# Optimization experiments

Measured on AMD Instinct MI355X. Metric: run time of the kernel, lower is better.

The kernel has to match this reference:

```python
import jax, jax.numpy as jnp
import numpy as np


def setup_inputs() -> dict:
    key = jax.random.key(0)
    ks = jax.random.split(key, 10)
    B, L, Din, Dout = 64, 512, 256, 256
    s = 0.05
    inp = jax.random.normal(ks[0], (B, L, Din), jnp.float32)
    ci = jax.random.randint(ks[1], (B, L), 0, L)
    # valid coref indices: ci[:, i] must be in [0, i] (refers to an already-produced state)
    ci = ci % (jnp.arange(L) + 1)[None, :]
    p = lambda k, sh: jax.random.normal(k, sh, jnp.float32) * s
    return {
        "inp": inp,
        "last_coref_idx": ci,
        "Wr": p(ks[2], (Din, Dout)), "br": jnp.zeros((Dout,), jnp.float32),
        "Ur": p(ks[3], (Dout, Dout)),
        "Wz": p(ks[4], (Din, Dout)), "bz": jnp.zeros((Dout,), jnp.float32),
        "Uz": p(ks[5], (Dout, Dout)),
        "Wh": p(ks[6], (Din, Dout)), "bh": jnp.zeros((Dout,), jnp.float32),
        "Uh": p(ks[7], (Dout, Dout)),
        "k1": p(ks[8], (Din, 1)),
        "k2": p(ks[9], (Din, 1)),
    }


def reference(inp, last_coref_idx, Wr, br, Ur, Wz, bz, Uz, Wh, bh, Uh, k1, k2):
    B, L, Din = inp.shape
    Dout = Wr.shape[1]
    split = Dout // 2
    bidx = jnp.arange(B)

    def step(carry, xs):
        h_last, hist = carry            # h_last [B,Dout], hist [L,B,Dout]
        x, c, i = xs                    # x [B,Din], c [B] int, i scalar step index
        # coref = state_history[c-1][b] if c > 0 else zeros
        coref = hist[jnp.clip(c - 1, 0), bidx]
        coref = jnp.where((c > 0)[:, None], coref, jnp.zeros_like(coref))
        # attention between h_last-half and coref-half
        e = jnp.concatenate([x @ k1, x @ k2], axis=1)      # [B,2]
        a = jax.nn.softmax(e, axis=1)[:, 0:1]              # [B,1]
        mt = jnp.concatenate([a * h_last[:, :split], (1.0 - a) * coref[:, split:]], axis=1)
        r = jax.nn.sigmoid(x @ Wr + br + mt @ Ur)
        z = jax.nn.sigmoid(x @ Wz + bz + mt @ Uz)
        h_ = jnp.tanh(x @ Wh + bh + r * (mt @ Uh))
        h = (1.0 - z) * mt + z * h_
        hist = jax.lax.dynamic_update_index_in_dim(hist, h, i, 0)
        return (h, hist), h

    h0 = jnp.zeros((B, Dout), inp.dtype)
    hist0 = jnp.zeros((L, B, Dout), inp.dtype)
    xs = (jnp.swapaxes(inp, 0, 1), jnp.swapaxes(last_coref_idx, 0, 1), jnp.arange(L))
    _, ys = jax.lax.scan(step, (h0, hist0), xs)            # ys [L,B,Dout]
    return jnp.swapaxes(ys, 0, 1)                          # [B,L,Dout]
```

## Files before the change

### kernel.cpp

```cpp
#include <hip/hip_runtime.h>
#include <stdint.h>
#include <stddef.h>

typedef _Float16 half_t;
typedef _Float16 half2_t __attribute__((ext_vector_type(2)));
typedef _Float16 half8_t __attribute__((ext_vector_type(8)));
typedef float    floatx4 __attribute__((ext_vector_type(4)));
typedef uint32_t u32x4   __attribute__((ext_vector_type(4)));

#define SEQ_L 512
#define NBATCH 64
#define DIM 256
#define NTOT (NBATCH * SEQ_L)

__device__ __forceinline__ float fdot2f(uint32_t a, uint32_t b, float c) {
#if defined(__has_builtin)
#if __has_builtin(__builtin_amdgcn_fdot2)
  return __builtin_amdgcn_fdot2(__builtin_bit_cast(half2_t, a),
                                __builtin_bit_cast(half2_t, b), c, false);
#else
  half2_t av = __builtin_bit_cast(half2_t, a);
  half2_t bv = __builtin_bit_cast(half2_t, b);
  return c + (float)av[0] * (float)bv[0] + (float)av[1] * (float)bv[1];
#endif
#else
  half2_t av = __builtin_bit_cast(half2_t, a);
  half2_t bv = __builtin_bit_cast(half2_t, b);
  return c + (float)av[0] * (float)bv[0] + (float)av[1] * (float)bv[1];
#endif
}

__device__ __forceinline__ float sigmoidf_fast(float x) {
  return 1.0f / (1.0f + __expf(-x));
}
__device__ __forceinline__ float tanhf_fast(float x) {
  float e = __expf(2.0f * x);
  return 1.0f - 2.0f / (e + 1.0f);
}

__global__ void conv_w_kernel(const float* __restrict__ Wr,
                              const float* __restrict__ Wz,
                              const float* __restrict__ Wh,
                              half_t* __restrict__ Wt) {
  int n = blockIdx.x;
  int k = threadIdx.x;
  const float* W = (n < 256) ? Wr : ((n < 512) ? Wz : Wh);
  int j = n & 255;
  Wt[(size_t)n * DIM + k] = (half_t)W[(size_t)k * DIM + j];
}

__global__ __launch_bounds__(256) void attn_a_kernel(const float* __restrict__ inp,
                                                     const float* __restrict__ k1,
                                                     const float* __restrict__ k2,
                                                     float* __restrict__ a_arr) {
  int row  = blockIdx.x * 4 + (threadIdx.x >> 6);
  int lane = threadIdx.x & 63;
  const float4* x4 = (const float4*)(inp + (size_t)row * DIM);
  float4 xv  = x4[lane];
  float4 k1v = ((const float4*)k1)[lane];
  float4 k2v = ((const float4*)k2)[lane];
  float e1 = xv.x * k1v.x + xv.y * k1v.y + xv.z * k1v.z + xv.w * k1v.w;
  float e2 = xv.x * k2v.x + xv.y * k2v.y + xv.z * k2v.z + xv.w * k2v.w;
#pragma unroll
  for (int off = 32; off >= 1; off >>= 1) {
    e1 += __shfl_xor(e1, off);
    e2 += __shfl_xor(e2, off);
  }
  if (lane == 0) a_arr[row] = 1.0f / (1.0f + __expf(e2 - e1));
}

__global__ __launch_bounds__(256) void gemm_p_kernel(const float* __restrict__ X,
                                                     const half_t* __restrict__ Wt,
                                                     half_t* __restrict__ P) {
  __shared__ __align__(16) half_t As[128][32];
  __shared__ __align__(16) half_t Bs[128][32];
  const int tid  = threadIdx.x;
  const int bm   = blockIdx.x * 128;
  const int bn   = blockIdx.y * 128;
  const int lane = tid & 63;
  const int wave = tid >> 6;
  const int wm   = (wave >> 1) * 64;
  const int wn   = (wave & 1) * 64;
  const int quad = lane >> 4;
  const int l15  = lane & 15;
  const int r0   = tid >> 2;
  const int kc   = (tid & 3) * 8;

  floatx4 acc[4][4] = {};

  for (int k0 = 0; k0 < DIM; k0 += 32) {
#pragma unroll
    for (int hh = 0; hh < 2; ++hh) {
      int r = r0 + hh * 64;
      const float* asrc = X + (size_t)(bm + r) * DIM + k0 + kc;
      float4 f0 = *(const float4*)(asrc);
      float4 f1 = *(const float4*)(asrc + 4);
      half8_t av;
      av[0] = (half_t)f0.x; av[1] = (half_t)f0.y; av[2] = (half_t)f0.z; av[3] = (half_t)f0.w;
      av[4] = (half_t)f1.x; av[5] = (half_t)f1.y; av[6] = (half_t)f1.z; av[7] = (half_t)f1.w;
      *(half8_t*)(&As[r][kc]) = av;
      *(half8_t*)(&Bs[r][kc]) = *(const half8_t*)(Wt + (size_t)(bn + r) * DIM + k0 + kc);
    }
    __syncthreads();
    half8_t af[4], bf[4];
#pragma unroll
    for (int mi = 0; mi < 4; ++mi)
      af[mi] = *(const half8_t*)(&As[wm + mi * 16 + l15][quad * 8]);
#pragma unroll
    for (int ni = 0; ni < 4; ++ni)
      bf[ni] = *(const half8_t*)(&Bs[wn + ni * 16 + l15][quad * 8]);
#pragma unroll
    for (int mi = 0; mi < 4; ++mi)
#pragma unroll
      for (int ni = 0; ni < 4; ++ni)
        acc[mi][ni] = __builtin_amdgcn_mfma_f32_16x16x32_f16(af[mi], bf[ni], acc[mi][ni], 0, 0, 0);
    __syncthreads();
  }
#pragma unroll
  for (int mi = 0; mi < 4; ++mi)
#pragma unroll
    for (int ni = 0; ni < 4; ++ni) {
      int col = bn + wn + ni * 16 + l15;
#pragma unroll
      for (int rr = 0; rr < 4; ++rr) {
        int row = bm + wm + mi * 16 + quad * 4 + rr;
        P[(size_t)row * 768 + col] = (half_t)acc[mi][ni][rr];
      }
    }
}

__global__ __launch_bounds__(512, 2) void recur_kernel(
    const half_t* __restrict__ P,
    const float* __restrict__ a_arr,
    const int* __restrict__ cidx,
    const float* __restrict__ Ur, const float* __restrict__ Uz, const float* __restrict__ Uh,
    const float* __restrict__ br, const float* __restrict__ bz, const float* __restrict__ bh,
    float* __restrict__ out) {
  const int b    = blockIdx.x;
  const int tid  = threadIdx.x;
  const int j    = tid & 255;
  const int half = tid >> 8;
  const int koff = half * 128;

  __shared__ __align__(16) half_t hist[SEQ_L][128];
  __shared__ __align__(16) half_t mth[DIM];
  __shared__ float part1[3][DIM];

  u32x4 ur4[16], uz4[16], uh4[16];
#pragma unroll
  for (int q = 0; q < 16; ++q) {
#pragma unroll
    for (int t = 0; t < 4; ++t) {
      const int k = koff + q * 8 + t * 2;
      half2_t tr, tz, th;
      tr[0] = (half_t)Ur[(size_t)(k + 0) * DIM + j];
      tr[1] = (half_t)Ur[(size_t)(k + 1) * DIM + j];
      tz[0] = (half_t)Uz[(size_t)(k + 0) * DIM + j];
      tz[1] = (half_t)Uz[(size_t)(k + 1) * DIM + j];
      th[0] = (half_t)Uh[(size_t)(k + 0) * DIM + j];
      th[1] = (half_t)Uh[(size_t)(k + 1) * DIM + j];
      ur4[q][t] = __builtin_bit_cast(uint32_t, tr);
      uz4[q][t] = __builtin_bit_cast(uint32_t, tz);
      uh4[q][t] = __builtin_bit_cast(uint32_t, th);
    }
  }
  const float brj = br[j], bzj = bz[j], bhj = bh[j];

  if (tid < 128) ((uint32_t*)mth)[tid] = 0u;
  __syncthreads();

  float h   = 0.0f;
  float mtj = 0.0f;
  const int base = b * SEQ_L;

  for (int i = 0; i < SEQ_L; ++i) {
    float pr = 0.f, pz = 0.f, ph = 0.f;
    if (half == 0) {
      const half_t* prow = P + (size_t)(base + i) * 768;
      pr = (float)prow[j];
      pz = (float)prow[DIM + j];
      ph = (float)prow[2 * DIM + j];
    }
    const bool  more   = (i + 1 < SEQ_L);
    const float a_next = more ? a_arr[base + i + 1] : 0.0f;
    const int   c_next = more ? cidx[base + i + 1]  : 0;

    float accr = 0.0f, accz = 0.0f, acch = 0.0f;
    const u32x4* mq = (const u32x4*)(mth + koff);
#pragma unroll
    for (int q = 0; q < 16; ++q) {
      u32x4 m4 = mq[q];
      accr = fdot2f(m4.x, ur4[q][0], accr);
      accr = fdot2f(m4.y, ur4[q][1], accr);
      accr = fdot2f(m4.z, ur4[q][2], accr);
      accr = fdot2f(m4.w, ur4[q][3], accr);
      accz = fdot2f(m4.x, uz4[q][0], accz);
      accz = fdot2f(m4.y, uz4[q][1], accz);
      accz = fdot2f(m4.z, uz4[q][2], accz);
      accz = fdot2f(m4.w, uz4[q][3], accz);
      acch = fdot2f(m4.x, uh4[q][0], acch);
      acch = fdot2f(m4.y, uh4[q][1], acch);
      acch = fdot2f(m4.z, uh4[q][2], acch);
      acch = fdot2f(m4.w, uh4[q][3], acch);
    }
    if (half == 1) {
      part1[0][j] = accr;
      part1[1][j] = accz;
      part1[2][j] = acch;
    }
    __syncthreads();

    if (half == 0) {
      accr += part1[0][j];
      accz += part1[1][j];
      acch += part1[2][j];
      const float rg = sigmoidf_fast(pr + brj + accr);
      const float zg = sigmoidf_fast(pz + bzj + accz);
      const float hb = tanhf_fast(ph + bhj + rg * acch);
      h = (1.0f - zg) * mtj + zg * hb;
      out[(size_t)(base + i) * DIM + j] = h;
      if (j >= 128) hist[i][j - 128] = (half_t)h;
      float mtn;
      if (j < 128) {
        mtn = a_next * h;
      } else {
        float coref = (c_next > 0) ? (float)hist[c_next - 1][j - 128] : 0.0f;
        mtn = (1.0f - a_next) * coref;
      }
      mtj = mtn;
      mth[j] = (half_t)mtn;
    }
    __syncthreads();
  }
}

extern "C" void kernel_launch(void* const* d_in, const int* in_sizes, int n_in,
                              void* d_out, int out_size, void* d_ws, size_t ws_size,
                              hipStream_t stream) {
  const float* inp = (const float*)d_in[0];
  const int*   ci  = (const int*)d_in[1];
  const float* Wr  = (const float*)d_in[2];
  const float* br  = (const float*)d_in[3];
  const float* Ur  = (const float*)d_in[4];
  const float* Wz  = (const float*)d_in[5];
  const float* bz  = (const float*)d_in[6];
  const float* Uz  = (const float*)d_in[7];
  const float* Wh  = (const float*)d_in[8];
  const float* bh  = (const float*)d_in[9];
  const float* Uh  = (const float*)d_in[10];
  const float* k1  = (const float*)d_in[11];
  const float* k2  = (const float*)d_in[12];
  float* out = (float*)d_out;

  char* ws = (char*)d_ws;
  half_t* Wt    = (half_t*)ws;
  half_t* P     = (half_t*)(ws + 393216);
  float*  a_arr = (float*)(ws + 393216 + 50331648);

  conv_w_kernel<<<dim3(768), dim3(256), 0, stream>>>(Wr, Wz, Wh, Wt);
  attn_a_kernel<<<dim3(NTOT / 4), dim3(256), 0, stream>>>(inp, k1, k2, a_arr);
  gemm_p_kernel<<<dim3(NTOT / 128, 6), dim3(256), 0, stream>>>(inp, Wt, P);
  recur_kernel<<<dim3(NBATCH), dim3(512), 0, stream>>>(P, a_arr, ci, Ur, Uz, Uh,
                                                       br, bz, bh, out);
}
```

Before: 822.7 us.

## Split recurrent matvec K dimension across four thread groups per batch

```diff
diff --git a/kernel.cpp b/kernel.cpp
--- a/kernel.cpp
+++ b/kernel.cpp
@@ -129,7 +129,7 @@
     }
 }
 
-__global__ __launch_bounds__(512, 2) void recur_kernel(
+__global__ __launch_bounds__(1024, 4) void recur_kernel(
     const half_t* __restrict__ P,
     const float* __restrict__ a_arr,
     const int* __restrict__ cidx,
@@ -139,19 +139,19 @@
   const int b    = blockIdx.x;
   const int tid  = threadIdx.x;
   const int j    = tid & 255;
-  const int half = tid >> 8;
-  const int koff = half * 128;
+  const int q    = tid >> 8;
+  const int koff = q * 64;
 
   __shared__ __align__(16) half_t hist[SEQ_L][128];
   __shared__ __align__(16) half_t mth[DIM];
-  __shared__ float part1[3][DIM];
-
-  u32x4 ur4[16], uz4[16], uh4[16];
-#pragma unroll
-  for (int q = 0; q < 16; ++q) {
+  __shared__ __align__(16) floatx4 part[3][DIM];
+
+  u32x4 ur4[8], uz4[8], uh4[8];
+#pragma unroll
+  for (int c8 = 0; c8 < 8; ++c8) {
 #pragma unroll
     for (int t = 0; t < 4; ++t) {
-      const int k = koff + q * 8 + t * 2;
+      const int k = koff + c8 * 8 + t * 2;
       half2_t tr, tz, th;
       tr[0] = (half_t)Ur[(size_t)(k + 0) * DIM + j];
       tr[1] = (half_t)Ur[(size_t)(k + 1) * DIM + j];
@@ -159,9 +159,9 @@
       tz[1] = (half_t)Uz[(size_t)(k + 1) * DIM + j];
       th[0] = (half_t)Uh[(size_t)(k + 0) * DIM + j];
       th[1] = (half_t)Uh[(size_t)(k + 1) * DIM + j];
-      ur4[q][t] = __builtin_bit_cast(uint32_t, tr);
-      uz4[q][t] = __builtin_bit_cast(uint32_t, tz);
-      uh4[q][t] = __builtin_bit_cast(uint32_t, th);
+      ur4[c8][t] = __builtin_bit_cast(uint32_t, tr);
+      uz4[c8][t] = __builtin_bit_cast(uint32_t, tz);
+      uh4[c8][t] = __builtin_bit_cast(uint32_t, th);
     }
   }
   const float brj = br[j], bzj = bz[j], bhj = bh[j];
@@ -175,45 +175,48 @@
 
   for (int i = 0; i < SEQ_L; ++i) {
     float pr = 0.f, pz = 0.f, ph = 0.f;
-    if (half == 0) {
+    if (q == 0) {
       const half_t* prow = P + (size_t)(base + i) * 768;
       pr = (float)prow[j];
       pz = (float)prow[DIM + j];
       ph = (float)prow[2 * DIM + j];
     }
-    const bool  more   = (i + 1 < SEQ_L);
-    const float a_next = more ? a_arr[base + i + 1] : 0.0f;
-    const int   c_next = more ? cidx[base + i + 1]  : 0;
+    const int   inext  = (i < SEQ_L - 1) ? (i + 1) : (SEQ_L - 1);
+    const float a_next = a_arr[base + inext];
+    const int   c_next = cidx[base + inext];
 
     float accr = 0.0f, accz = 0.0f, acch = 0.0f;
     const u32x4* mq = (const u32x4*)(mth + koff);
 #pragma unroll
-    for (int q = 0; q < 16; ++q) {
-      u32x4 m4 = mq[q];
-      accr = fdot2f(m4.x, ur4[q][0], accr);
-      accr = fdot2f(m4.y, ur4[q][1], accr);
-      accr = fdot2f(m4.z, ur4[q][2], accr);
-      accr = fdot2f(m4.w, ur4[q][3], accr);
-      accz = fdot2f(m4.x, uz4[q][0], accz);
-      accz = fdot2f(m4.y, uz4[q][1], accz);
-      accz = fdot2f(m4.z, uz4[q][2], accz);
-      accz = fdot2f(m4.w, uz4[q][3], accz);
-      acch = fdot2f(m4.x, uh4[q][0], acch);
-      acch = fdot2f(m4.y, uh4[q][1], acch);
-      acch = fdot2f(m4.z, uh4[q][2], acch);
-      acch = fdot2f(m4.w, uh4[q][3], acch);
-    }
-    if (half == 1) {
-      part1[0][j] = accr;
-      part1[1][j] = accz;
-      part1[2][j] = acch;
-    }
-    __syncthreads();
-
-    if (half == 0) {
-      accr += part1[0][j];
-      accz += part1[1][j];
-      acch += part1[2][j];
+    for (int c8 = 0; c8 < 8; ++c8) {
+      u32x4 m4 = mq[c8];
+      accr = fdot2f(m4.x, ur4[c8][0], accr);
+      accz = fdot2f(m4.x, uz4[c8][0], accz);
+      acch = fdot2f(m4.x, uh4[c8][0], acch);
+      accr = fdot2f(m4.y, ur4[c8][1], accr);
+      accz = fdot2f(m4.y, uz4[c8][1], accz);
+      acch = fdot2f(m4.y, uh4[c8][1], acch);
+      accr = fdot2f(m4.z, ur4[c8][2], accr);
+      accz = fdot2f(m4.z, uz4[c8][2], accz);
+      acch = fdot2f(m4.z, uh4[c8][2], acch);
+      accr = fdot2f(m4.w, ur4[c8][3], accr);
+      accz = fdot2f(m4.w, uz4[c8][3], accz);
+      acch = fdot2f(m4.w, uh4[c8][3], acch);
+    }
+    if (q > 0) {
+      floatx4 p;
+      p[0] = accr; p[1] = accz; p[2] = acch; p[3] = 0.0f;
+      part[q - 1][j] = p;
+    }
+    __syncthreads();
+
+    if (q == 0) {
+      floatx4 p0 = part[0][j];
+      floatx4 p1 = part[1][j];
+      floatx4 p2 = part[2][j];
+      accr += p0[0] + p1[0] + p2[0];
+      accz += p0[1] + p1[1] + p2[1];
+      acch += p0[2] + p1[2] + p2[2];
       const float rg = sigmoidf_fast(pr + brj + accr);
       const float zg = sigmoidf_fast(pz + bzj + accz);
       const float hb = tanhf_fast(ph + bhj + rg * acch);
@@ -260,6 +263,6 @@
   conv_w_kernel<<<dim3(768), dim3(256), 0, stream>>>(Wr, Wz, Wh, Wt);
   attn_a_kernel<<<dim3(NTOT / 4), dim3(256), 0, stream>>>(inp, k1, k2, a_arr);
   gemm_p_kernel<<<dim3(NTOT / 128, 6), dim3(256), 0, stream>>>(inp, Wt, P);
-  recur_kernel<<<dim3(NBATCH), dim3(512), 0, stream>>>(P, a_arr, ci, Ur, Uz, Uh,
-                                                       br, bz, bh, out);
-}
+  recur_kernel<<<dim3(NBATCH), dim3(1024), 0, stream>>>(P, a_arr, ci, Ur, Uz, Uh,
+                                                        br, bz, bh, out);
+}
```

Result: slower. 964.4 us (+17.2%).
